# Kernel optimization log

Measured on AMD Instinct MI355X. Metric: run time of the kernel, lower is better.

Reference implementation:

```python
import jax, jax.numpy as jnp
import numpy as np
import math

DIM = 1024
THETA = 10000.0


def rope_cos_sin(seq_len, dim, dtype=jnp.float32):
    # freqs over pairs: 1/theta^(2i/dim), angles = t * freq
    inv = 1.0 / (THETA ** (jnp.arange(0, dim, 2, dtype=jnp.float32) / dim))  # [dim/2]
    t = jnp.arange(seq_len, dtype=jnp.float32)
    ang = jnp.outer(t, inv)  # [S, dim/2]
    return jnp.cos(ang).astype(dtype), jnp.sin(ang).astype(dtype)


def apply_rotary(x, cos, sin):
    # x: [B, S, D]; treat consecutive pairs as complex (xr + i*xi)
    B, S, D = x.shape
    xr = x[..., 0::2]  # [B, S, D/2]
    xi = x[..., 1::2]
    or_ = xr * cos - xi * sin
    oi_ = xr * sin + xi * cos
    # interleave back: (..., D/2, 2) -> (..., D)
    return jnp.stack([or_, oi_], axis=-1).reshape(B, S, D)


def setup_inputs() -> dict:
    key = jax.random.key(0)
    ks = jax.random.split(key, 5)
    B, S, D = 4, 2048, DIM
    x = jax.random.normal(ks[0], (B, S, D), dtype=jnp.float32)
    s = 1.0 / math.sqrt(D)
    wq = jax.random.normal(ks[1], (D, D), dtype=jnp.float32) * s
    wk = jax.random.normal(ks[2], (D, D), dtype=jnp.float32) * s
    wv = jax.random.normal(ks[3], (D, D), dtype=jnp.float32) * s
    wo = jax.random.normal(ks[4], (D, D), dtype=jnp.float32) * s
    return {"x": x, "wq": wq, "wk": wk, "wv": wv, "wo": wo}


def reference(x, wq, wk, wv, wo):
    B, S, D = x.shape
    xq = jnp.einsum('bsd,ed->bse', x, wq)  # Linear: x @ W^T
    xk = jnp.einsum('bsd,ed->bse', x, wk)
    xv = jnp.einsum('bsd,ed->bse', x, wv)
    cos, sin = rope_cos_sin(S, D, x.dtype)
    xq = apply_rotary(xq, cos, sin)
    xk = apply_rotary(xk, cos, sin)
    scores = jnp.einsum('bqd,bkd->bqk', xq, xk) / jnp.sqrt(jnp.asarray(D, x.dtype))
    attn = jax.nn.softmax(scores, axis=-1)  # no causal mask in original
    out = jnp.einsum('bqk,bkd->bqd', attn, xv)
    return jnp.einsum('bsd,ed->bse', out, wo)
```

## Files before the change

### kernel.cpp

```cpp
#include <hip/hip_runtime.h>
#include <math.h>

typedef __attribute__((ext_vector_type(8))) short short8;
typedef __attribute__((ext_vector_type(4))) float f32x4;
typedef unsigned short u16;

__device__ __forceinline__ float b2f(u16 u) {
    union { unsigned u; float f; } c; c.u = ((unsigned)u) << 16; return c.f;
}
__device__ __forceinline__ u16 f2b(float f) {
    unsigned u = __float_as_uint(f);
    u += 0x7fffu + ((u >> 16) & 1u);
    return (u16)(u >> 16);
}

__device__ __forceinline__ void gl_lds16(const u16* g, u16* l) {
    __builtin_amdgcn_global_load_lds(
        (const __attribute__((address_space(1))) void*)g,
        (__attribute__((address_space(3))) void*)l,
        16, 0, 0);
}

__global__ __launch_bounds__(256) void cvt_f32_bf16(const float* __restrict__ src,
                                                    u16* __restrict__ dst, int n) {
    const int i = (blockIdx.x * 256 + threadIdx.x) * 8;
    if (i >= n) return;
    const float4 a = *(const float4*)&src[i];
    const float4 b = *(const float4*)&src[i + 4];
    short8 o;
    o[0] = (short)f2b(a.x); o[1] = (short)f2b(a.y);
    o[2] = (short)f2b(a.z); o[3] = (short)f2b(a.w);
    o[4] = (short)f2b(b.x); o[5] = (short)f2b(b.y);
    o[6] = (short)f2b(b.z); o[7] = (short)f2b(b.w);
    *(short8*)&dst[i] = o;
}

__global__ __launch_bounds__(256) void cvt_weights(
    const float* __restrict__ w0, const float* __restrict__ w1,
    const float* __restrict__ w2, const float* __restrict__ w3,
    u16* __restrict__ dst) {
    const int z = blockIdx.z;
    const float* src = (z == 0) ? w0 : (z == 1) ? w1 : (z == 2) ? w2 : w3;
    const int i = (blockIdx.x * 256 + threadIdx.x) * 8;
    const float4 a = *(const float4*)&src[i];
    const float4 b = *(const float4*)&src[i + 4];
    short8 o;
    o[0] = (short)f2b(a.x); o[1] = (short)f2b(a.y);
    o[2] = (short)f2b(a.z); o[3] = (short)f2b(a.w);
    o[4] = (short)f2b(b.x); o[5] = (short)f2b(b.y);
    o[6] = (short)f2b(b.z); o[7] = (short)f2b(b.w);
    *(short8*)&dst[(long)z * 1024 * 1024 + i] = o;
}

template<typename OT>
__device__ __forceinline__ void gemm_body(
    const u16* __restrict__ A, const u16* __restrict__ W, OT* __restrict__ C,
    int lda, int ldw, int ldc, int K, float scale)
{
    __shared__ u16 lsA[128 * 32];
    __shared__ u16 lsB[128 * 32];

    const int m0 = blockIdx.y * 128;
    const int n0 = blockIdx.x * 128;
    const int t = threadIdx.x;
    const int lane = t & 63;
    const int wave = t >> 6;
    const int wm = (wave & 1) * 64;
    const int wn = (wave >> 1) * 64;

    const int sr = t >> 2;
    const int scol = ((t & 3) ^ ((t >> 3) & 3)) * 8;

    const u16* pa0 = A + (long)(m0 + sr) * lda + scol;
    const u16* pa1 = pa0 + (long)64 * lda;
    const u16* pw0 = W + (long)(n0 + sr) * ldw + scol;
    const u16* pw1 = pw0 + (long)64 * ldw;
    u16* const la0 = &lsA[t * 8];
    u16* const la1 = &lsA[2048 + t * 8];
    u16* const lb0 = &lsB[t * 8];
    u16* const lb1 = &lsB[2048 + t * 8];

    f32x4 acc[4][4];
#pragma unroll
    for (int i = 0; i < 4; ++i)
#pragma unroll
        for (int j = 0; j < 4; ++j)
            acc[i][j] = (f32x4){0.f, 0.f, 0.f, 0.f};

    const int fr = lane & 15;
    const int fq = lane >> 4;
    const int aoff = (wm + fr) * 32 + (fq ^ ((fr >> 1) & 3)) * 8;
    const int boff = (wn + fr) * 32 + (fq ^ ((fr >> 1) & 3)) * 8;

    for (int k0 = 0; k0 < K; k0 += 32) {
        __syncthreads();
        gl_lds16(pa0, la0); pa0 += 32;
        gl_lds16(pa1, la1); pa1 += 32;
        gl_lds16(pw0, lb0); pw0 += 32;
        gl_lds16(pw1, lb1); pw1 += 32;
        __syncthreads();

        short8 af[4], bf[4];
#pragma unroll
        for (int i = 0; i < 4; ++i)
            af[i] = *(const short8*)&lsA[aoff + i * 512];
#pragma unroll
        for (int j = 0; j < 4; ++j)
            bf[j] = *(const short8*)&lsB[boff + j * 512];
#pragma unroll
        for (int i = 0; i < 4; ++i)
#pragma unroll
            for (int j = 0; j < 4; ++j)
                acc[i][j] = __builtin_amdgcn_mfma_f32_16x16x32_bf16(af[i], bf[j], acc[i][j], 0, 0, 0);
    }

#pragma unroll
    for (int i = 0; i < 4; ++i) {
#pragma unroll
        for (int j = 0; j < 4; ++j) {
            const int row0 = m0 + wm + i * 16 + fq * 4;
            const int col = n0 + wn + j * 16 + fr;
#pragma unroll
            for (int r = 0; r < 4; ++r) {
                const int row = row0 + r;
                const float val = acc[i][j][r] * scale;
                if (sizeof(OT) == 2) {
                    ((u16*)C)[(long)row * ldc + col] = f2b(val);
                } else {
                    ((float*)C)[(long)row * ldc + col] = val;
                }
            }
        }
    }
}

template<typename OT>
__global__ __launch_bounds__(256) void gemm_bt(
    const u16* __restrict__ A, const u16* __restrict__ W, OT* __restrict__ C,
    int lda, int ldw, int ldc, int K,
    long sA, long sW, long sC, float scale)
{
    const int bz = blockIdx.z;
    gemm_body<OT>(A + (long)bz * sA, W + (long)bz * sW, C + (long)bz * sC,
                  lda, ldw, ldc, K, scale);
}

__global__ __launch_bounds__(256) void gemm_dual(
    const u16* __restrict__ A0, const u16* __restrict__ W0, u16* __restrict__ C0,
    int lda0, int ldw0, int ldc0, long sA0, long sW0, long sC0, float scale0,
    const u16* __restrict__ A1, const u16* __restrict__ W1, u16* __restrict__ C1,
    int lda1, int ldw1, int ldc1, long sA1, long sW1, long sC1, float scale1)
{
    const int z = blockIdx.z;
    if (z < 4) {
        gemm_body<u16>(A0 + (long)z * sA0, W0 + (long)z * sW0, C0 + (long)z * sC0,
                       lda0, ldw0, ldc0, 1024, scale0);
    } else {
        if (blockIdx.y >= 8) return;
        const int b = z - 4;
        gemm_body<u16>(A1 + (long)b * sA1, W1 + (long)b * sW1, C1 + (long)b * sC1,
                       lda1, ldw1, ldc1, 1024, scale1);
    }
}

__global__ __launch_bounds__(256) void rope_kernel(u16* q, u16* k) {
    const int row = blockIdx.x;
    const int pos = row & 2047;
    u16* p = (blockIdx.y ? k : q) + (long)row * 1024;
#pragma unroll
    for (int it = 0; it < 2; ++it) {
        const int i = threadIdx.x + it * 256;
        const float e = (float)i * (1.0f / 512.0f);
        const float inv = powf(10000.0f, -e);
        const float ang = (float)pos * inv;
        float s, c;
        sincosf(ang, &s, &c);
        const float xr = b2f(p[2 * i]);
        const float xi = b2f(p[2 * i + 1]);
        p[2 * i]     = f2b(xr * c - xi * s);
        p[2 * i + 1] = f2b(xr * s + xi * c);
    }
}

__global__ __launch_bounds__(256) void softmax_kernel(const u16* __restrict__ S, u16* __restrict__ P) {
    const long row = blockIdx.x;
    const u16* src = S + row * 2048;
    u16* dst = P + row * 2048;
    const int t = threadIdx.x;
    const int lane = t & 63;
    const int wave = t >> 6;
    __shared__ float red[4];

    float v[8];
    const short8 raw = *(const short8*)&src[t * 8];
#pragma unroll
    for (int i = 0; i < 8; ++i) v[i] = b2f((u16)raw[i]);

    float m = v[0];
#pragma unroll
    for (int i = 1; i < 8; ++i) m = fmaxf(m, v[i]);
    for (int o = 32; o > 0; o >>= 1) m = fmaxf(m, __shfl_xor(m, o, 64));
    if (lane == 0) red[wave] = m;
    __syncthreads();
    m = fmaxf(fmaxf(red[0], red[1]), fmaxf(red[2], red[3]));
    __syncthreads();

    float sum = 0.f;
#pragma unroll
    for (int i = 0; i < 8; ++i) { v[i] = expf(v[i] - m); sum += v[i]; }
    for (int o = 32; o > 0; o >>= 1) sum += __shfl_xor(sum, o, 64);
    if (lane == 0) red[wave] = sum;
    __syncthreads();
    sum = red[0] + red[1] + red[2] + red[3];
    const float is = 1.0f / sum;

    short8 outv;
#pragma unroll
    for (int i = 0; i < 8; ++i) outv[i] = (short)f2b(v[i] * is);
    *(short8*)&dst[t * 8] = outv;
}

extern "C" void kernel_launch(void* const* d_in, const int* in_sizes, int n_in,
                              void* d_out, int out_size, void* d_ws, size_t ws_size,
                              hipStream_t stream)
{
    (void)in_sizes; (void)n_in; (void)out_size; (void)ws_size;
    const float* x  = (const float*)d_in[0];
    const float* wq = (const float*)d_in[1];
    const float* wk = (const float*)d_in[2];
    const float* wv = (const float*)d_in[3];
    const float* wo = (const float*)d_in[4];
    float* out = (float*)d_out;

    const long M1 = 1024 * 1024;
    u16* ws  = (u16*)d_ws;
    u16* xb  = ws;
    u16* wqb = xb + 8 * M1;
    u16* wob = wqb + 3 * M1;
    u16* q   = wqb + 4 * M1;
    u16* kk  = q + 8 * M1;
    u16* v   = kk + 8 * M1;
    u16* sc  = v + 8 * M1;
    u16* UT  = xb;

    const dim3 blk(256);

    cvt_f32_bf16<<<dim3(4096), blk, 0, stream>>>(x, xb, 8 * 1024 * 1024);
    cvt_weights<<<dim3(512, 1, 4), blk, 0, stream>>>(wq, wk, wv, wo, wqb);

    gemm_bt<u16><<<dim3(8, 64, 3), blk, 0, stream>>>(xb, wqb, q,
        1024, 1024, 1024, 1024, 0, M1, 8 * M1, 1.0f);

    rope_kernel<<<dim3(8192, 2), blk, 0, stream>>>(q, kk);

    gemm_dual<<<dim3(16, 16, 8), blk, 0, stream>>>(
        q, kk, sc, 1024, 1024, 2048, 2 * M1, 2 * M1, 4 * M1, 0.03125f,
        wob, v, UT, 1024, 1024, 2048, 0, 2 * M1, 2 * M1, 1.0f);

    softmax_kernel<<<dim3(8192), blk, 0, stream>>>(sc, sc);

    gemm_bt<float><<<dim3(8, 16, 4), blk, 0, stream>>>(sc, UT, out,
        2048, 2048, 1024, 2048, 4 * M1, 2 * M1, 2 * M1, 1.0f);
}
```

Before: 339.2 us.

## Double-buffer LDS tiles in GEMM to overlap global loads with MFMA

Splits the GEMM's shared-memory A and B tiles into two buffers. The next K-slice is prefetched with global_load_lds into the idle buffer while MFMAs run on the current one, which drops one of the two barriers per iteration. The aim is to hide global-memory latency behind compute. It doubles LDS use per block, which may lower occupancy, and the compiler may still insert conservative vmcnt waits before the LDS reads, which would cancel the overlap.

Measured after the change: 326.6 us. 1.04x faster.

```diff
diff --git a/kernel.cpp b/kernel.cpp
--- a/kernel.cpp
+++ b/kernel.cpp
@@ -57,8 +57,8 @@
     const u16* __restrict__ A, const u16* __restrict__ W, OT* __restrict__ C,
     int lda, int ldw, int ldc, int K, float scale)
 {
-    __shared__ u16 lsA[128 * 32];
-    __shared__ u16 lsB[128 * 32];
+    __shared__ u16 lsA[2][128 * 32];
+    __shared__ u16 lsB[2][128 * 32];
 
     const int m0 = blockIdx.y * 128;
     const int n0 = blockIdx.x * 128;
@@ -75,10 +75,6 @@
     const u16* pa1 = pa0 + (long)64 * lda;
     const u16* pw0 = W + (long)(n0 + sr) * ldw + scol;
     const u16* pw1 = pw0 + (long)64 * ldw;
-    u16* const la0 = &lsA[t * 8];
-    u16* const la1 = &lsA[2048 + t * 8];
-    u16* const lb0 = &lsB[t * 8];
-    u16* const lb1 = &lsB[2048 + t * 8];
 
     f32x4 acc[4][4];
 #pragma unroll
@@ -89,29 +85,40 @@
 
     const int fr = lane & 15;
     const int fq = lane >> 4;
-    const int aoff = (wm + fr) * 32 + (fq ^ ((fr >> 1) & 3)) * 8;
-    const int boff = (wn + fr) * 32 + (fq ^ ((fr >> 1) & 3)) * 8;
-
-    for (int k0 = 0; k0 < K; k0 += 32) {
+    const int swz = (fq ^ ((fr >> 1) & 3)) * 8;
+    const int aoff = (wm + fr) * 32 + swz;
+    const int boff = (wn + fr) * 32 + swz;
+
+    gl_lds16(pa0, &lsA[0][t * 8]);        pa0 += 32;
+    gl_lds16(pa1, &lsA[0][2048 + t * 8]); pa1 += 32;
+    gl_lds16(pw0, &lsB[0][t * 8]);        pw0 += 32;
+    gl_lds16(pw1, &lsB[0][2048 + t * 8]); pw1 += 32;
+
+    const int nsteps = K >> 5;
+    int par = 0;
+    for (int s = 0; s < nsteps; ++s) {
         __syncthreads();
-        gl_lds16(pa0, la0); pa0 += 32;
-        gl_lds16(pa1, la1); pa1 += 32;
-        gl_lds16(pw0, lb0); pw0 += 32;
-        gl_lds16(pw1, lb1); pw1 += 32;
-        __syncthreads();
+        if (s + 1 < nsteps) {
+            const int np = par ^ 1;
+            gl_lds16(pa0, &lsA[np][t * 8]);        pa0 += 32;
+            gl_lds16(pa1, &lsA[np][2048 + t * 8]); pa1 += 32;
+            gl_lds16(pw0, &lsB[np][t * 8]);        pw0 += 32;
+            gl_lds16(pw1, &lsB[np][2048 + t * 8]); pw1 += 32;
+        }
 
         short8 af[4], bf[4];
 #pragma unroll
         for (int i = 0; i < 4; ++i)
-            af[i] = *(const short8*)&lsA[aoff + i * 512];
+            af[i] = *(const short8*)&lsA[par][aoff + i * 512];
 #pragma unroll
         for (int j = 0; j < 4; ++j)
-            bf[j] = *(const short8*)&lsB[boff + j * 512];
+            bf[j] = *(const short8*)&lsB[par][boff + j * 512];
 #pragma unroll
         for (int i = 0; i < 4; ++i)
 #pragma unroll
             for (int j = 0; j < 4; ++j)
                 acc[i][j] = __builtin_amdgcn_mfma_f32_16x16x32_bf16(af[i], bf[j], acc[i][j], 0, 0, 0);
+        par ^= 1;
     }
 
 #pragma unroll
```
